# Optimization experiments

Hardware: AMD Instinct MI355X
Metric: run time of the kernel (lower is better)

The kernel has to match this reference:

```python
import jax, jax.numpy as jnp
import numpy as np

N, C1, C2, M, B, TOPK = 8192, 512, 128, 4, 256, 40
EPS = 1e-5


def setup_inputs() -> dict:
    key = jax.random.key(0)
    ks = jax.random.split(key, 8)
    s = 1.0 / np.sqrt(C2)
    return {
        "x": jax.random.normal(ks[0], (B, C1), jnp.float32),
        "embedding": jax.random.normal(ks[1], (N, C2), jnp.float32),
        "Wq": jax.random.uniform(ks[2], (M * C2, C2), jnp.float32, -s, s),
        "bq": jax.random.uniform(ks[3], (M * C2,), jnp.float32, -s, s),
        "Wv": jax.random.uniform(ks[4], (C2, C2), jnp.float32, -s, s),
        "bv": jax.random.uniform(ks[5], (C2,), jnp.float32, -s, s),
        "bn1_gamma": jnp.ones((C2,), jnp.float32),
        "bn1_beta": jnp.zeros((C2,), jnp.float32),
        "ln_gamma": jnp.ones((C2,), jnp.float32),
        "ln_beta": jnp.zeros((C2,), jnp.float32),
    }


def _perm_table():
    # torch.manual_seed(seed); torch.randperm(N) with seed in {0,1,2,3} ->
    # 4 fixed permutations. We use jax-native seeded permutations (same structure,
    # different concrete permutation values than torch's RNG).
    return jnp.stack([jax.random.permutation(jax.random.key(s), N) for s in range(4)])


def reference(x, embedding, Wq, bq, Wv, bv, bn1_gamma, bn1_beta, ln_gamma, ln_beta):
    # q path: [B, M, C2] -> to_q -> [B, M, M*C2] -> BN over C2 -> [B, M*M, C2]
    q = x.reshape(B, M, C2) @ Wq.T + bq                      # [B, M, M*C2]
    q = q.reshape(-1, C2)                                    # [B*M*M, C2]
    mu = q.mean(axis=0)
    var = q.var(axis=0)                                      # biased, like torch BN training
    q = (q - mu) / jnp.sqrt(var + EPS) * bn1_gamma + bn1_beta
    q = q.reshape(B, M * M, C2)

    v = embedding @ Wv.T + bv                                # [N, C2]
    kmu = embedding.mean(axis=-1, keepdims=True)
    kvar = embedding.var(axis=-1, keepdims=True)
    k = (embedding - kmu) / jnp.sqrt(kvar + EPS) * ln_gamma + ln_beta  # LN [N, C2]
    # torch does k.view(-1, c2, N) on contiguous [B, N, c2]: a raw RESHAPE, not transpose.
    k = k.reshape(C2, N)

    attn = jnp.einsum('bqc,cn->bqn', q, k) / jnp.sqrt(jnp.float32(C2))  # [B, M*M, N]
    attn = jax.nn.softmax(attn, axis=-1)
    applied = jnp.einsum('bqn,nc->bqc', attn, v)             # [B, M*M, C2]

    topv, topi = jax.lax.top_k(attn, TOPK)                   # [B, M*M, TOPK]
    bidx = jnp.arange(B)[:, None, None]
    qidx = jnp.arange(M * M)[None, :, None]
    masked = jnp.zeros_like(attn).at[bidx, qidx, topi].set(topv)

    avg = topi.reshape(B, -1).astype(jnp.float32).mean(axis=-1)
    seed = jnp.floor(avg / (N / 4.0)).astype(jnp.int32) % 4  # in {0..3}
    perms = _perm_table()[seed]                              # [B, N]
    idx = jnp.broadcast_to(perms[:, None, :], masked.shape)
    attn_w = jnp.take_along_axis(masked, idx, axis=-1)       # per-sample column permutation

    attn_w_flat = attn_w.reshape(B, -1)
    applied_flat = applied.reshape(B, -1)
    # matches torch return (attn_weights, x_s=[q, attn_applied], attn_applied)
    return attn_w_flat, q, applied, applied_flat
```

## Files before the change

### kernel.cpp

```cpp
#include <hip/hip_runtime.h>
#include <hip/hip_bf16.h>
#include <stdint.h>

#define EPSF 1e-5f

typedef __bf16 b16x8 __attribute__((ext_vector_type(8)));
typedef float f32x4 __attribute__((ext_vector_type(4)));
typedef unsigned short u16x8 __attribute__((ext_vector_type(8)));

static __device__ __forceinline__ unsigned short f2bf(float f) {
  __hip_bfloat16 h = __float2bfloat16(f);
  return __builtin_bit_cast(unsigned short, h);
}

__device__ __forceinline__ void threefry2x32(uint32_t k0, uint32_t k1,
                                             uint32_t c0, uint32_t c1,
                                             uint32_t& o0, uint32_t& o1) {
  const uint32_t ks2 = k0 ^ k1 ^ 0x1BD11BDAu;
  uint32_t x0 = c0 + k0, x1 = c1 + k1;
#define TFR(r) { x0 += x1; x1 = (x1 << (r)) | (x1 >> (32 - (r))); x1 ^= x0; }
  TFR(13) TFR(15) TFR(26) TFR(6)
  x0 += k1;  x1 += ks2 + 1u;
  TFR(17) TFR(29) TFR(16) TFR(24)
  x0 += ks2; x1 += k0 + 2u;
  TFR(13) TFR(15) TFR(26) TFR(6)
  x0 += k0;  x1 += k1 + 3u;
  TFR(17) TFR(29) TFR(16) TFR(24)
  x0 += k1;  x1 += ks2 + 4u;
  TFR(13) TFR(15) TFR(26) TFR(6)
  x0 += ks2; x1 += k0 + 5u;
#undef TFR
  o0 = x0; o1 = x1;
}

__global__ __launch_bounds__(256) void rank_kernel(int* __restrict__ rankbuf) {
  __shared__ uint32_t bits[8192];
  const int chunk = blockIdx.x;
  const int round = blockIdx.y;
  const int s     = blockIdx.z;
  const int t = threadIdx.x, l = t & 63, w = t >> 6;
  uint32_t ka, kb;
  {
    uint32_t k1a, k1b;
    threefry2x32(0u, (uint32_t)s, 0u, 0u, k1a, k1b);
    if (round == 0) threefry2x32(0u, (uint32_t)s, 0u, 1u, ka, kb);
    else            threefry2x32(k1a, k1b, 0u, 1u, ka, kb);
  }
  for (int j = t; j < 8192; j += 256) {
    uint32_t t0, t1;
    threefry2x32(ka, kb, 0u, (uint32_t)j, t0, t1);
    bits[j] = t1;
  }
  __syncthreads();
  const int base = chunk * 256 + w * 64;
  const int i = base + l;
  const uint32_t myb = bits[i];
  const uint4* b4 = (const uint4*)bits;
  int rk = 0;
  const int lo = base >> 2;
#pragma unroll 4
  for (int j4 = 0; j4 < lo; j4++) {
    const uint4 b = b4[j4];
    rk += (b.x <= myb) + (b.y <= myb) + (b.z <= myb) + (b.w <= myb);
  }
#pragma unroll
  for (int j4 = lo; j4 < lo + 16; j4++) {
    const uint4 b = b4[j4];
    const int j = j4 * 4;
    rk += (b.x < myb) + ((b.x == myb) && (j     < i));
    rk += (b.y < myb) + ((b.y == myb) && (j + 1 < i));
    rk += (b.z < myb) + ((b.z == myb) && (j + 2 < i));
    rk += (b.w < myb) + ((b.w == myb) && (j + 3 < i));
  }
#pragma unroll 4
  for (int j4 = lo + 16; j4 < 2048; j4++) {
    const uint4 b = b4[j4];
    rk += (b.x < myb) + (b.y < myb) + (b.z < myb) + (b.w < myb);
  }
  rankbuf[(s * 2 + round) * 8192 + i] = rk;
}

__global__ __launch_bounds__(256) void compose_kernel(const int* __restrict__ rankbuf,
                                                      int* __restrict__ invperm) {
  const int s = blockIdx.y;
  const int v = blockIdx.x * 256 + threadIdx.x;
  const int* r1 = rankbuf + s * 16384;
  const int* r2 = r1 + 8192;
  invperm[s * 8192 + v] = r2[r1[v]];
}

__global__ __launch_bounds__(256) void qraw_kernel(const float* __restrict__ x,
    const float* __restrict__ Wq, const float* __restrict__ bq,
    float* __restrict__ qraw) {
  __shared__ float ea[16][128];
  __shared__ float wq[128][132];
  const int t = threadIdx.x;
  const int g = blockIdx.x;
  const int m2 = blockIdx.y;
  for (int i = t; i < 512; i += 256) {
    float4 xx = *(const float4*)(x + (size_t)g * 2048 + i * 4);
    *(float4*)&ea[i >> 5][(i & 31) * 4] = xx;
  }
  for (int i = t; i < 4096; i += 256) {
    float4 ww = *(const float4*)(Wq + (size_t)m2 * 16384 + i * 4);
    *(float4*)&wq[i >> 5][(i & 31) * 4] = ww;
  }
  __syncthreads();
  const int row = t >> 4, j = t & 15;
  float acc[8] = {0.f,0.f,0.f,0.f,0.f,0.f,0.f,0.f};
  for (int d = 0; d < 128; d++) {
    const float xv = ea[row][d];
#pragma unroll
    for (int cc = 0; cc < 8; cc++) acc[cc] += xv * wq[j + cc * 16][d];
  }
  const int r = (g * 16 + row) * 4 + m2;
#pragma unroll
  for (int cc = 0; cc < 8; cc++) {
    const int c = j + cc * 16;
    qraw[(size_t)r * 128 + c] = acc[cc] + bq[m2 * 128 + c];
  }
}

__global__ __launch_bounds__(256) void bnpart_kernel(const float* __restrict__ qraw,
                                                     float* __restrict__ bnpart) {
  __shared__ float a1[256], a2[256];
  const int t = threadIdx.x, c = t & 127, h = t >> 7;
  float s1 = 0.f, s2 = 0.f;
  for (int i = 0; i < 64; i++) {
    float xv = qraw[(size_t)(blockIdx.x * 128 + h + 2 * i) * 128 + c];
    s1 += xv; s2 += xv * xv;
  }
  a1[t] = s1; a2[t] = s2;
  __syncthreads();
  if (t < 128) {
    bnpart[blockIdx.x * 256 + t]       = a1[t] + a1[t + 128];
    bnpart[blockIdx.x * 256 + 128 + t] = a2[t] + a2[t + 128];
  }
}

__global__ void bnfin_kernel(const float* __restrict__ bnpart,
                             const float* __restrict__ gamma,
                             const float* __restrict__ beta,
                             float* __restrict__ bnstat) {
  const int c = threadIdx.x;
  float s1 = 0.f, s2 = 0.f;
  for (int i = 0; i < 32; i++) { s1 += bnpart[i * 256 + c]; s2 += bnpart[i * 256 + 128 + c]; }
  const float mu  = s1 * (1.0f / 4096.0f);
  const float var = s2 * (1.0f / 4096.0f) - mu * mu;
  const float sc  = rsqrtf(var + EPSF) * gamma[c];
  bnstat[c]       = sc;
  bnstat[128 + c] = beta[c] - mu * sc;
}

__global__ __launch_bounds__(256) void qnorm_kernel(const float* __restrict__ qraw,
    const float* __restrict__ bnstat, float* __restrict__ outq,
    unsigned short* __restrict__ qb) {
  const int idx4 = blockIdx.x * 256 + threadIdx.x;
  float4 xv = *(const float4*)(qraw + (size_t)idx4 * 4);
  const int c0 = (idx4 * 4) & 127;
  float4 sc = *(const float4*)(bnstat + c0);
  float4 sh = *(const float4*)(bnstat + 128 + c0);
  float4 o;
  o.x = xv.x * sc.x + sh.x; o.y = xv.y * sc.y + sh.y;
  o.z = xv.z * sc.z + sh.z; o.w = xv.w * sc.w + sh.w;
  *(float4*)(outq + (size_t)idx4 * 4) = o;
  ushort4 ob;
  ob.x = f2bf(o.x); ob.y = f2bf(o.y); ob.z = f2bf(o.z); ob.w = f2bf(o.w);
  *(ushort4*)(qb + (size_t)idx4 * 4) = ob;
}

__global__ __launch_bounds__(256) void lnv_kernel(const float* __restrict__ emb,
    const float* __restrict__ Wv, const float* __restrict__ bv,
    const float* __restrict__ lng, const float* __restrict__ lnb,
    float* __restrict__ kbuf, float* __restrict__ vbuf) {
  __shared__ float ea[16][128];
  __shared__ float wv[128][132];
  const int t = threadIdx.x;
  const int r0 = blockIdx.x * 16;
  for (int i = t; i < 512; i += 256) {
    float4 xx = *(const float4*)(emb + (size_t)r0 * 128 + i * 4);
    *(float4*)&ea[i >> 5][(i & 31) * 4] = xx;
  }
  for (int i = t; i < 4096; i += 256) {
    float4 ww = *(const float4*)(Wv + (size_t)i * 4);
    *(float4*)&wv[i >> 5][(i & 31) * 4] = ww;
  }
  __syncthreads();
  const int row = t >> 4, j = t & 15;
  float s1 = 0.f, s2 = 0.f;
#pragma unroll
  for (int m = 0; m < 8; m++) { float xv = ea[row][j + m * 16]; s1 += xv; s2 += xv * xv; }
#pragma unroll
  for (int off = 8; off; off >>= 1) {
    s1 += __shfl_xor(s1, off, 16);
    s2 += __shfl_xor(s2, off, 16);
  }
  const float mu   = s1 * 0.0078125f;
  const float var  = s2 * 0.0078125f - mu * mu;
  const float rstd = rsqrtf(var + EPSF);
#pragma unroll
  for (int m = 0; m < 8; m++) {
    const int d = j + m * 16;
    kbuf[(size_t)(r0 + row) * 128 + d] = (ea[row][d] - mu) * rstd * lng[d] + lnb[d];
  }
  float acc[8] = {0.f,0.f,0.f,0.f,0.f,0.f,0.f,0.f};
  for (int d = 0; d < 128; d++) {
    const float xv = ea[row][d];
#pragma unroll
    for (int cc = 0; cc < 8; cc++) acc[cc] += xv * wv[j + cc * 16][d];
  }
#pragma unroll
  for (int cc = 0; cc < 8; cc++) {
    const int c = j + cc * 16;
    vbuf[(size_t)(r0 + row) * 128 + c] = acc[cc] + bv[c];
  }
}

__global__ __launch_bounds__(256) void ktrans_kernel(const float* __restrict__ kbuf,
                                                     unsigned short* __restrict__ kT) {
  __shared__ unsigned short s[64][136];
  const int b = blockIdx.x, t = threadIdx.x;
  const int k = t >> 1, half = t & 1;
  const float* src = kbuf + (size_t)(k * 64 + (b >> 1)) * 128 + (b & 1) * 64 + half * 32;
#pragma unroll
  for (int i = 0; i < 8; i++) {
    float4 v = *(const float4*)(src + i * 4);
    const int dn = half * 32 + i * 4;
    s[dn + 0][k] = f2bf(v.x); s[dn + 1][k] = f2bf(v.y);
    s[dn + 2][k] = f2bf(v.z); s[dn + 3][k] = f2bf(v.w);
  }
  __syncthreads();
  const int dn = t >> 2, q = t & 3;
  unsigned short* dst = kT + (size_t)(b * 64 + dn) * 128 + q * 32;
#pragma unroll
  for (int j = 0; j < 4; j++)
    *(int4*)(dst + j * 8) = *(const int4*)&s[dn][q * 32 + j * 8];
}

__global__ __launch_bounds__(256) void vtrans_kernel(const float* __restrict__ vbuf,
                                                     unsigned short* __restrict__ vT) {
  __shared__ unsigned short s[128][72];
  const int b = blockIdx.x, t = threadIdx.x;
  const int i0 = b * 64;
  const int di = t >> 2, q = t & 3;
  const float* src = vbuf + (size_t)(i0 + di) * 128 + q * 32;
#pragma unroll
  for (int i = 0; i < 8; i++) {
    float4 v = *(const float4*)(src + i * 4);
    const int c = q * 32 + i * 4;
    s[c + 0][di] = f2bf(v.x); s[c + 1][di] = f2bf(v.y);
    s[c + 2][di] = f2bf(v.z); s[c + 3][di] = f2bf(v.w);
  }
  __syncthreads();
  const int c = t >> 1, half = t & 1;
  unsigned short* dst = vT + (size_t)c * 8192 + i0 + half * 32;
#pragma unroll
  for (int j = 0; j < 4; j++)
    *(int4*)(dst + j * 8) = *(const int4*)&s[c][half * 32 + j * 8];
}

__global__ __launch_bounds__(256) void gemm1_mfma(const unsigned short* __restrict__ qb,
    const unsigned short* __restrict__ kT, float* __restrict__ logits) {
  __shared__ __attribute__((aligned(16))) unsigned short lds[32768];
  unsigned short* At = lds;
  unsigned short* Bt = lds + 16384;
  const int t = threadIdx.x, l = t & 63, w = t >> 6;
  const int n0 = blockIdx.x * 128, r0 = blockIdx.y * 128;
  const int wr = w >> 1, wc = w & 1;
#pragma unroll
  for (int it = 0; it < 8; it++) {
    const int c = it * 256 + t;
    const int row = c >> 4, ch = c & 15;
    const int chs = ch ^ (row & 7);
    const unsigned short* gA = qb + (size_t)(r0 + row) * 128 + chs * 8;
    const unsigned short* gB = kT + (size_t)(n0 + row) * 128 + chs * 8;
    __builtin_amdgcn_global_load_lds((const __attribute__((address_space(1))) void*)gA,
        (__attribute__((address_space(3))) void*)(At + (size_t)(it * 256 + w * 64) * 8), 16, 0, 0);
    __builtin_amdgcn_global_load_lds((const __attribute__((address_space(1))) void*)gB,
        (__attribute__((address_space(3))) void*)(Bt + (size_t)(it * 256 + w * 64) * 8), 16, 0, 0);
  }
  __syncthreads();
  f32x4 acc[4][4];
#pragma unroll
  for (int i = 0; i < 4; i++)
#pragma unroll
    for (int j = 0; j < 4; j++) acc[i][j] = (f32x4){0.f, 0.f, 0.f, 0.f};
#pragma unroll
  for (int ks = 0; ks < 4; ks++) {
    b16x8 af[4], bf[4];
#pragma unroll
    for (int i = 0; i < 4; i++) {
      const int rl = wr * 64 + i * 16 + (l & 15);
      const int ch = (ks * 4 + (l >> 4)) ^ (rl & 7);
      af[i] = __builtin_bit_cast(b16x8, *(const u16x8*)&At[rl * 128 + ch * 8]);
    }
#pragma unroll
    for (int j = 0; j < 4; j++) {
      const int cl = wc * 64 + j * 16 + (l & 15);
      const int ch = (ks * 4 + (l >> 4)) ^ (cl & 7);
      bf[j] = __builtin_bit_cast(b16x8, *(const u16x8*)&Bt[cl * 128 + ch * 8]);
    }
#pragma unroll
    for (int i = 0; i < 4; i++)
#pragma unroll
      for (int j = 0; j < 4; j++)
        acc[i][j] = __builtin_amdgcn_mfma_f32_16x16x32_bf16(af[i], bf[j], acc[i][j], 0, 0, 0);
  }
  __syncthreads();
  float* fb = (float*)lds;
  const float rs = 0.08838834764831845f;
#pragma unroll
  for (int i = 0; i < 4; i++)
#pragma unroll
    for (int j = 0; j < 4; j++) {
#pragma unroll
      for (int jj = 0; jj < 4; jj++) {
        const int row = wr * 64 + i * 16 + (l >> 4) * 4 + jj;
        const int col = wc * 64 + j * 16 + (l & 15);
        fb[row * 128 + col] = acc[i][j][jj] * rs;
      }
    }
  __syncthreads();
#pragma unroll
  for (int kk = 0; kk < 16; kk++) {
    const int idx4 = kk * 256 + t;
    const int row = idx4 >> 5, c4 = idx4 & 31;
    *(float4*)(logits + (size_t)(r0 + row) * 8192 + n0 + c4 * 4) = *(const float4*)&fb[row * 128 + c4 * 4];
  }
}

__global__ __launch_bounds__(256) void rowstat_topk_kernel(const float* __restrict__ logits,
    float* __restrict__ rowmax, float* __restrict__ rowsum,
    float* __restrict__ topv, int* __restrict__ topi) {
  const int r = blockIdx.x, t = threadIdx.x;
  const int l = t & 63, w = t >> 6;
  const float* row = logits + (size_t)r * 8192;
  float4 v[8];
#pragma unroll
  for (int m = 0; m < 8; m++) v[m] = *(const float4*)(row + m * 1024 + t * 4);

  __shared__ float sredf[4];
  __shared__ int scnt[16];
  __shared__ unsigned long long keys[1024];
  __shared__ int lcnt;

  float bm = -3.0e38f;
#pragma unroll
  for (int m = 0; m < 8; m++)
    bm = fmaxf(bm, fmaxf(fmaxf(v[m].x, v[m].y), fmaxf(v[m].z, v[m].w)));
#pragma unroll
  for (int off = 32; off; off >>= 1) bm = fmaxf(bm, __shfl_xor(bm, off));
  if (l == 0) sredf[w] = bm;
  __syncthreads();
  const float gmax = fmaxf(fmaxf(sredf[0], sredf[1]), fmaxf(sredf[2], sredf[3]));

  float ls = 0.f;
#pragma unroll
  for (int m = 0; m < 8; m++)
    ls += expf(v[m].x - gmax) + expf(v[m].y - gmax) + expf(v[m].z - gmax) + expf(v[m].w - gmax);
#pragma unroll
  for (int off = 32; off; off >>= 1) ls += __shfl_xor(ls, off);
  __syncthreads();
  if (l == 0) sredf[w] = ls;
  __syncthreads();
  const float gsum = sredf[0] + sredf[1] + sredf[2] + sredf[3];
  if (t == 0) { rowmax[r] = gmax; rowsum[r] = gsum; }

  float theta = -3.0e38f;
  bool found = false;
  for (int trial = 0; trial < 8 && !found; trial++) {
    const float base = gmax - 8.0f * (float)trial;
    int c[16];
#pragma unroll
    for (int j = 0; j < 16; j++) c[j] = 0;
#pragma unroll
    for (int m = 0; m < 8; m++) {
#pragma unroll
      for (int j = 0; j < 16; j++) {
        const float th = base - 0.5f * (float)(j + 1);
        c[j] += (v[m].x >= th) + (v[m].y >= th) + (v[m].z >= th) + (v[m].w >= th);
      }
    }
#pragma unroll
    for (int j = 0; j < 16; j++) {
#pragma unroll
      for (int off = 32; off; off >>= 1) c[j] += __shfl_xor(c[j], off);
    }
    if (t < 16) scnt[t] = 0;
    __syncthreads();
    if (l == 0) {
#pragma unroll
      for (int j = 0; j < 16; j++) atomicAdd(&scnt[j], c[j]);
    }
    __syncthreads();
    for (int j = 0; j < 16; j++) {
      if (scnt[j] >= 40) { theta = base - 0.5f * (float)(j + 1); found = true; break; }
    }
    __syncthreads();
  }

  if (t == 0) lcnt = 0;
  __syncthreads();
#pragma unroll
  for (int m = 0; m < 8; m++) {
    const int gb = m * 1024 + t * 4;
    const float vals[4] = {v[m].x, v[m].y, v[m].z, v[m].w};
#pragma unroll
    for (int e = 0; e < 4; e++) {
      if (vals[e] >= theta) {
        const int pos = atomicAdd(&lcnt, 1);
        if (pos < 1024) {
          const uint32_t s = __float_as_uint(vals[e]);
          const uint32_t mkey = (s & 0x80000000u) ? ~s : (s | 0x80000000u);
          keys[pos] = ((unsigned long long)(~mkey) << 32) | (unsigned)(gb + e);
        }
      }
    }
  }
  __syncthreads();
  const int cnt = min(lcnt, 1024);
  const float rgs = 1.0f / gsum;
  for (int i = t; i < cnt; i += 256) {
    const unsigned long long K = keys[i];
    int rank = 0;
#pragma unroll 4
    for (int p = 0; p < cnt; p++) rank += (keys[p] < K) ? 1 : 0;
    if (rank < 40) {
      const uint32_t desc = (uint32_t)(K >> 32);
      const uint32_t mkey = ~desc;
      const uint32_t sb = (mkey & 0x80000000u) ? (mkey & 0x7FFFFFFFu) : ~mkey;
      const float val = __uint_as_float(sb);
      topi[r * 40 + rank] = (int)(K & 0xFFFFFFFFu);
      topv[r * 40 + rank] = expf(val - gmax) * rgs;
    }
  }
}

__global__ __launch_bounds__(256) void gemm2_mfma(const float* __restrict__ logits,
    const unsigned short* __restrict__ vT, const float* __restrict__ rowmax,
    const float* __restrict__ rowsum, float* __restrict__ pvpart) {
  __shared__ __attribute__((aligned(16))) unsigned short lds[32768];
  unsigned short* At = lds;
  unsigned short* Bt = lds + 8192;
  const int t = threadIdx.x, l = t & 63, w = t >> 6;
  const int bx = blockIdx.x;
  const int by = blockIdx.y;
  const int r0 = by * 128;
  const int kb0 = bx * 1024;
  const int wr = w >> 1, wc = w & 1;
  const int prow = t >> 1, pk = (t & 1) * 32;
  const float rm = rowmax[r0 + prow];
  const float ri = 1.0f / rowsum[r0 + prow];

  f32x4 acc[4][4];
#pragma unroll
  for (int i = 0; i < 4; i++)
#pragma unroll
    for (int j = 0; j < 4; j++) acc[i][j] = (f32x4){0.f, 0.f, 0.f, 0.f};

  for (int ks = 0; ks < 16; ks++) {
    const int k0 = kb0 + ks * 64;
    __syncthreads();
#pragma unroll
    for (int it = 0; it < 4; it++) {
      const int c = it * 256 + t;
      const int rowc = c >> 3, ch = c & 7;
      const int chs = ch ^ (rowc & 7);
      const unsigned short* gB = vT + (size_t)rowc * 8192 + k0 + chs * 8;
      __builtin_amdgcn_global_load_lds((const __attribute__((address_space(1))) void*)gB,
          (__attribute__((address_space(3))) void*)(Bt + (size_t)(it * 256 + w * 64) * 8), 16, 0, 0);
    }
    const float* lsrc = logits + (size_t)(r0 + prow) * 8192 + k0 + pk;
#pragma unroll
    for (int c8 = 0; c8 < 4; c8++) {
      float4 v0 = *(const float4*)(lsrc + c8 * 8);
      float4 v1 = *(const float4*)(lsrc + c8 * 8 + 4);
      u16x8 pkd;
      pkd[0] = f2bf(expf(v0.x - rm) * ri); pkd[1] = f2bf(expf(v0.y - rm) * ri);
      pkd[2] = f2bf(expf(v0.z - rm) * ri); pkd[3] = f2bf(expf(v0.w - rm) * ri);
      pkd[4] = f2bf(expf(v1.x - rm) * ri); pkd[5] = f2bf(expf(v1.y - rm) * ri);
      pkd[6] = f2bf(expf(v1.z - rm) * ri); pkd[7] = f2bf(expf(v1.w - rm) * ri);
      const int chunkidx = (t & 1) * 4 + c8;
      const int phys = chunkidx ^ (prow & 7);
      *(u16x8*)&At[prow * 64 + phys * 8] = pkd;
    }
    __syncthreads();
#pragma unroll
    for (int s = 0; s < 2; s++) {
      b16x8 af[4], bf[4];
#pragma unroll
      for (int i = 0; i < 4; i++) {
        const int rl = wr * 64 + i * 16 + (l & 15);
        const int ch = (s * 4 + (l >> 4)) ^ (rl & 7);
        af[i] = __builtin_bit_cast(b16x8, *(const u16x8*)&At[rl * 64 + ch * 8]);
      }
#pragma unroll
      for (int j = 0; j < 4; j++) {
        const int cl = wc * 64 + j * 16 + (l & 15);
        const int ch = (s * 4 + (l >> 4)) ^ (cl & 7);
        bf[j] = __builtin_bit_cast(b16x8, *(const u16x8*)&Bt[cl * 64 + ch * 8]);
      }
#pragma unroll
      for (int i = 0; i < 4; i++)
#pragma unroll
        for (int j = 0; j < 4; j++)
          acc[i][j] = __builtin_amdgcn_mfma_f32_16x16x32_bf16(af[i], bf[j], acc[i][j], 0, 0, 0);
    }
  }
  __syncthreads();
  float* fb = (float*)lds;
#pragma unroll
  for (int i = 0; i < 4; i++)
#pragma unroll
    for (int j = 0; j < 4; j++)
#pragma unroll
      for (int jj = 0; jj < 4; jj++) {
        const int row = wr * 64 + i * 16 + (l >> 4) * 4 + jj;
        const int col = wc * 64 + j * 16 + (l & 15);
        fb[row * 128 + col] = acc[i][j][jj];
      }
  __syncthreads();
#pragma unroll
  for (int kk = 0; kk < 16; kk++) {
    const int idx4 = kk * 256 + t;
    const int row = idx4 >> 5, c4 = idx4 & 31;
    *(float4*)(pvpart + ((size_t)bx * 4096 + r0 + row) * 128 + c4 * 4) = *(const float4*)&fb[row * 128 + c4 * 4];
  }
}

__global__ __launch_bounds__(256) void pvred_kernel(const float* __restrict__ pvpart,
    float* __restrict__ o2, float* __restrict__ o3) {
  const int idx4 = blockIdx.x * 256 + threadIdx.x;
  float4 s; s.x = s.y = s.z = s.w = 0.f;
#pragma unroll
  for (int ch = 0; ch < 8; ch++) {
    float4 p = *(const float4*)(pvpart + (size_t)ch * 524288 + (size_t)idx4 * 4);
    s.x += p.x; s.y += p.y; s.z += p.z; s.w += p.w;
  }
  *(float4*)(o2 + (size_t)idx4 * 4) = s;
  *(float4*)(o3 + (size_t)idx4 * 4) = s;
}

__global__ __launch_bounds__(256) void seedscatter_kernel(const int* __restrict__ topi,
    const float* __restrict__ topv, const int* __restrict__ invperm,
    float* __restrict__ out0) {
  const int b = blockIdx.x, t = threadIdx.x;
  int s = 0;
  for (int e = t; e < 640; e += 256) s += topi[b * 640 + e];
#pragma unroll
  for (int off = 32; off; off >>= 1) s += __shfl_xor(s, off);
  __shared__ int sred[4];
  if ((t & 63) == 0) sred[t >> 6] = s;
  __syncthreads();
  const int total = sred[0] + sred[1] + sred[2] + sred[3];
  const float avg = (float)total / 640.0f;
  const int sd = ((int)floorf(avg / 2048.0f)) & 3;
  const int* ip = invperm + sd * 8192;
  for (int e = t; e < 640; e += 256) {
    const int q = e / 40;
    const int i = topi[b * 640 + e];
    const float val = topv[b * 640 + e];
    out0[((size_t)(b * 16 + q)) * 8192 + ip[i]] = val;
  }
}

extern "C" void kernel_launch(void* const* d_in, const int* in_sizes, int n_in,
                              void* d_out, int out_size, void* d_ws, size_t ws_size,
                              hipStream_t stream) {
  const float* x   = (const float*)d_in[0];
  const float* emb = (const float*)d_in[1];
  const float* Wq  = (const float*)d_in[2];
  const float* bq  = (const float*)d_in[3];
  const float* Wv  = (const float*)d_in[4];
  const float* bv  = (const float*)d_in[5];
  const float* bng = (const float*)d_in[6];
  const float* bnb = (const float*)d_in[7];
  const float* lng = (const float*)d_in[8];
  const float* lnb = (const float*)d_in[9];

  float* out0  = (float*)d_out;
  float* outq  = out0 + 33554432;
  float* outap = outq + 524288;
  float* outaf = outap + 524288;

  float* wsf    = (float*)d_ws;
  float* kbuf   = wsf;
  float* vbuf   = kbuf + 1048576;
  float* qraw   = vbuf + 1048576;
  float* bnpart = qraw + 524288;
  float* bnstat = bnpart + 8192;
  float* rowmax = bnstat + 256;
  float* rowsum = rowmax + 4096;
  float* pvpart = rowsum + 4096;
  float* topv   = pvpart + 4194304;
  int*   topi    = (int*)(topv + 163840);
  int*   invperm = topi + 163840;
  int*   rankbuf = invperm + 32768;
  unsigned short* qb = (unsigned short*)(rankbuf + 65536);
  unsigned short* kT = qb + 524288;
  unsigned short* vT = kT + 1048576;

  rank_kernel<<<dim3(32, 2, 4), 256, 0, stream>>>(rankbuf);
  compose_kernel<<<dim3(32, 4), 256, 0, stream>>>(rankbuf, invperm);
  qraw_kernel<<<dim3(64, 4), 256, 0, stream>>>(x, Wq, bq, qraw);
  bnpart_kernel<<<32, 256, 0, stream>>>(qraw, bnpart);
  bnfin_kernel<<<1, 128, 0, stream>>>(bnpart, bng, bnb, bnstat);
  qnorm_kernel<<<512, 256, 0, stream>>>(qraw, bnstat, outq, qb);
  lnv_kernel<<<512, 256, 0, stream>>>(emb, Wv, bv, lng, lnb, kbuf, vbuf);
  ktrans_kernel<<<128, 256, 0, stream>>>(kbuf, kT);
  vtrans_kernel<<<128, 256, 0, stream>>>(vbuf, vT);
  gemm1_mfma<<<dim3(64, 32), 256, 0, stream>>>(qb, kT, out0);
  rowstat_topk_kernel<<<4096, 256, 0, stream>>>(out0, rowmax, rowsum, topv, topi);
  gemm2_mfma<<<dim3(8, 32), 256, 0, stream>>>(out0, vT, rowmax, rowsum, pvpart);
  pvred_kernel<<<512, 256, 0, stream>>>(pvpart, outap, outaf);
  hipMemsetAsync(d_out, 0, (size_t)33554432 * 4, stream);
  seedscatter_kernel<<<256, 256, 0, stream>>>(topi, topv, invperm, out0);
}
```

Measured before the change: 419.2 us.

## Fuse QK logits, softmax, PV and top-k candidate collection into flash-style kernels

```diff
diff --git a/kernel.cpp b/kernel.cpp
--- a/kernel.cpp
+++ b/kernel.cpp
@@ -3,6 +3,7 @@
 #include <stdint.h>
 
 #define EPSF 1e-5f
+#define RSQ 0.08838834764831845f
 
 typedef __bf16 b16x8 __attribute__((ext_vector_type(8)));
 typedef float f32x4 __attribute__((ext_vector_type(4)));
@@ -11,6 +12,9 @@
 static __device__ __forceinline__ unsigned short f2bf(float f) {
   __hip_bfloat16 h = __float2bfloat16(f);
   return __builtin_bit_cast(unsigned short, h);
+}
+static __device__ __forceinline__ float bf2f(unsigned short u) {
+  union { unsigned int i; float f; } x; x.i = ((unsigned int)u) << 16; return x.f;
 }
 
 __device__ __forceinline__ void threefry2x32(uint32_t k0, uint32_t k1,
@@ -216,327 +220,440 @@
   }
 }
 
-__global__ __launch_bounds__(256) void ktrans_kernel(const float* __restrict__ kbuf,
-                                                     unsigned short* __restrict__ kT) {
-  __shared__ unsigned short s[64][136];
+__global__ __launch_bounds__(256) void kvtrans_kernel(const float* __restrict__ kbuf,
+    const float* __restrict__ vbuf, unsigned short* __restrict__ kT,
+    unsigned short* __restrict__ vT) {
+  __shared__ __attribute__((aligned(16))) unsigned short sbuf[9216];
   const int b = blockIdx.x, t = threadIdx.x;
-  const int k = t >> 1, half = t & 1;
-  const float* src = kbuf + (size_t)(k * 64 + (b >> 1)) * 128 + (b & 1) * 64 + half * 32;
-#pragma unroll
-  for (int i = 0; i < 8; i++) {
-    float4 v = *(const float4*)(src + i * 4);
-    const int dn = half * 32 + i * 4;
-    s[dn + 0][k] = f2bf(v.x); s[dn + 1][k] = f2bf(v.y);
-    s[dn + 2][k] = f2bf(v.z); s[dn + 3][k] = f2bf(v.w);
-  }
-  __syncthreads();
-  const int dn = t >> 2, q = t & 3;
-  unsigned short* dst = kT + (size_t)(b * 64 + dn) * 128 + q * 32;
-#pragma unroll
-  for (int j = 0; j < 4; j++)
-    *(int4*)(dst + j * 8) = *(const int4*)&s[dn][q * 32 + j * 8];
-}
-
-__global__ __launch_bounds__(256) void vtrans_kernel(const float* __restrict__ vbuf,
-                                                     unsigned short* __restrict__ vT) {
-  __shared__ unsigned short s[128][72];
-  const int b = blockIdx.x, t = threadIdx.x;
-  const int i0 = b * 64;
-  const int di = t >> 2, q = t & 3;
-  const float* src = vbuf + (size_t)(i0 + di) * 128 + q * 32;
-#pragma unroll
-  for (int i = 0; i < 8; i++) {
-    float4 v = *(const float4*)(src + i * 4);
-    const int c = q * 32 + i * 4;
-    s[c + 0][di] = f2bf(v.x); s[c + 1][di] = f2bf(v.y);
-    s[c + 2][di] = f2bf(v.z); s[c + 3][di] = f2bf(v.w);
-  }
-  __syncthreads();
-  const int c = t >> 1, half = t & 1;
-  unsigned short* dst = vT + (size_t)c * 8192 + i0 + half * 32;
-#pragma unroll
-  for (int j = 0; j < 4; j++)
-    *(int4*)(dst + j * 8) = *(const int4*)&s[c][half * 32 + j * 8];
-}
-
-__global__ __launch_bounds__(256) void gemm1_mfma(const unsigned short* __restrict__ qb,
-    const unsigned short* __restrict__ kT, float* __restrict__ logits) {
+  if (blockIdx.y == 0) {
+    unsigned short (*s)[136] = (unsigned short (*)[136])sbuf;
+    const int k = t >> 1, half = t & 1;
+    const float* src = kbuf + (size_t)(k * 64 + (b >> 1)) * 128 + (b & 1) * 64 + half * 32;
+#pragma unroll
+    for (int i = 0; i < 8; i++) {
+      float4 v = *(const float4*)(src + i * 4);
+      const int dn = half * 32 + i * 4;
+      s[dn + 0][k] = f2bf(v.x); s[dn + 1][k] = f2bf(v.y);
+      s[dn + 2][k] = f2bf(v.z); s[dn + 3][k] = f2bf(v.w);
+    }
+    __syncthreads();
+    const int dn = t >> 2, q = t & 3;
+    unsigned short* dst = kT + (size_t)(b * 64 + dn) * 128 + q * 32;
+#pragma unroll
+    for (int j = 0; j < 4; j++)
+      *(int4*)(dst + j * 8) = *(const int4*)&s[dn][q * 32 + j * 8];
+  } else {
+    unsigned short (*s)[72] = (unsigned short (*)[72])sbuf;
+    const int i0 = b * 64;
+    const int di = t >> 2, q = t & 3;
+    const float* src = vbuf + (size_t)(i0 + di) * 128 + q * 32;
+#pragma unroll
+    for (int i = 0; i < 8; i++) {
+      float4 v = *(const float4*)(src + i * 4);
+      const int c = q * 32 + i * 4;
+      s[c + 0][di] = f2bf(v.x); s[c + 1][di] = f2bf(v.y);
+      s[c + 2][di] = f2bf(v.z); s[c + 3][di] = f2bf(v.w);
+    }
+    __syncthreads();
+    const int c = t >> 1, half = t & 1;
+    unsigned short* dst = vT + (size_t)c * 8192 + i0 + half * 32;
+#pragma unroll
+    for (int j = 0; j < 4; j++)
+      *(int4*)(dst + j * 8) = *(const int4*)&s[c][half * 32 + j * 8];
+  }
+}
+
+__global__ __launch_bounds__(512) void stats1_kernel(const unsigned short* __restrict__ qb,
+    const unsigned short* __restrict__ kT, float* __restrict__ maxpart) {
+  __shared__ __attribute__((aligned(16))) unsigned short ktt[16384];
+  __shared__ float red[128][4];
+  const int t = threadIdx.x, l = t & 63, w = t >> 6;
+  const int bx = blockIdx.x;
+  const int r0 = blockIdx.y * 128;
+  const int n0 = bx * 1024;
+  const int wr = w >> 2, wcol = w & 3;
+  b16x8 afr[4][4];
+#pragma unroll
+  for (int i = 0; i < 4; i++) {
+    const int rl = r0 + wr * 64 + i * 16 + (l & 15);
+#pragma unroll
+    for (int ks = 0; ks < 4; ks++)
+      afr[i][ks] = __builtin_bit_cast(b16x8,
+          *(const u16x8*)(qb + (size_t)rl * 128 + ks * 32 + (l >> 4) * 8));
+  }
+  float m16[4][4];
+#pragma unroll
+  for (int i = 0; i < 4; i++)
+#pragma unroll
+    for (int jj = 0; jj < 4; jj++) m16[i][jj] = -3.0e38f;
+
+  for (int ct = 0; ct < 8; ct++) {
+    __syncthreads();
+#pragma unroll
+    for (int it = 0; it < 4; it++) {
+      const int c = it * 512 + t;
+      const int row = c >> 4, ch = c & 15;
+      const int chs = ch ^ (row & 7);
+      const unsigned short* g = kT + (size_t)(n0 + ct * 128 + row) * 128 + chs * 8;
+      __builtin_amdgcn_global_load_lds((const __attribute__((address_space(1))) void*)g,
+          (__attribute__((address_space(3))) void*)(ktt + (size_t)(it * 512 + w * 64) * 8), 16, 0, 0);
+    }
+    __syncthreads();
+    f32x4 sacc[4][2];
+#pragma unroll
+    for (int i = 0; i < 4; i++)
+#pragma unroll
+      for (int j = 0; j < 2; j++) sacc[i][j] = (f32x4){0.f, 0.f, 0.f, 0.f};
+#pragma unroll
+    for (int ks = 0; ks < 4; ks++) {
+      b16x8 bf[2];
+#pragma unroll
+      for (int j = 0; j < 2; j++) {
+        const int cl = wcol * 32 + j * 16 + (l & 15);
+        const int ch = (ks * 4 + (l >> 4)) ^ (cl & 7);
+        bf[j] = __builtin_bit_cast(b16x8, *(const u16x8*)&ktt[cl * 128 + ch * 8]);
+      }
+#pragma unroll
+      for (int i = 0; i < 4; i++)
+#pragma unroll
+        for (int j = 0; j < 2; j++)
+          sacc[i][j] = __builtin_amdgcn_mfma_f32_16x16x32_bf16(afr[i][ks], bf[j], sacc[i][j], 0, 0, 0);
+    }
+#pragma unroll
+    for (int i = 0; i < 4; i++)
+#pragma unroll
+      for (int jj = 0; jj < 4; jj++)
+        m16[i][jj] = fmaxf(m16[i][jj], fmaxf(sacc[i][0][jj], sacc[i][1][jj]));
+  }
+#pragma unroll
+  for (int i = 0; i < 4; i++)
+#pragma unroll
+    for (int jj = 0; jj < 4; jj++) {
+      float m = m16[i][jj];
+#pragma unroll
+      for (int off = 8; off; off >>= 1) m = fmaxf(m, __shfl_xor(m, off));
+      if ((l & 15) == 0) red[wr * 64 + i * 16 + (l >> 4) * 4 + jj][wcol] = m;
+    }
+  __syncthreads();
+  if (t < 128)
+    maxpart[bx * 4096 + r0 + t] =
+        fmaxf(fmaxf(red[t][0], red[t][1]), fmaxf(red[t][2], red[t][3]));
+}
+
+__global__ __launch_bounds__(256) void rowmax_fin_kernel(const float* __restrict__ maxpart,
+                                                         float* __restrict__ rowmax) {
+  const int idx = blockIdx.x * 256 + threadIdx.x;
+  float m = -3.0e38f;
+#pragma unroll
+  for (int c = 0; c < 8; c++) m = fmaxf(m, maxpart[c * 4096 + idx]);
+  rowmax[idx] = m * RSQ;
+}
+
+__global__ __launch_bounds__(512) void fused2_kernel(const unsigned short* __restrict__ qb,
+    const unsigned short* __restrict__ kT, const unsigned short* __restrict__ vT,
+    const float* __restrict__ rowmax, float* __restrict__ pvpart,
+    float* __restrict__ expsumpart, unsigned long long* __restrict__ candbuf,
+    int* __restrict__ cnt) {
   __shared__ __attribute__((aligned(16))) unsigned short lds[32768];
-  unsigned short* At = lds;
-  unsigned short* Bt = lds + 16384;
+  unsigned short* kvt = lds;
+  unsigned short* pt  = lds + 16384;
   const int t = threadIdx.x, l = t & 63, w = t >> 6;
-  const int n0 = blockIdx.x * 128, r0 = blockIdx.y * 128;
-  const int wr = w >> 1, wc = w & 1;
-#pragma unroll
-  for (int it = 0; it < 8; it++) {
-    const int c = it * 256 + t;
-    const int row = c >> 4, ch = c & 15;
-    const int chs = ch ^ (row & 7);
-    const unsigned short* gA = qb + (size_t)(r0 + row) * 128 + chs * 8;
-    const unsigned short* gB = kT + (size_t)(n0 + row) * 128 + chs * 8;
-    __builtin_amdgcn_global_load_lds((const __attribute__((address_space(1))) void*)gA,
-        (__attribute__((address_space(3))) void*)(At + (size_t)(it * 256 + w * 64) * 8), 16, 0, 0);
-    __builtin_amdgcn_global_load_lds((const __attribute__((address_space(1))) void*)gB,
-        (__attribute__((address_space(3))) void*)(Bt + (size_t)(it * 256 + w * 64) * 8), 16, 0, 0);
-  }
-  __syncthreads();
-  f32x4 acc[4][4];
+  const int bx = blockIdx.x;
+  const int r0 = blockIdx.y * 128;
+  const int n0 = bx * 1024;
+  const int wr = w >> 2, wcol = w & 3;
+  b16x8 afr[4][4];
+#pragma unroll
+  for (int i = 0; i < 4; i++) {
+    const int rl = r0 + wr * 64 + i * 16 + (l & 15);
+#pragma unroll
+    for (int ks = 0; ks < 4; ks++)
+      afr[i][ks] = __builtin_bit_cast(b16x8,
+          *(const u16x8*)(qb + (size_t)rl * 128 + ks * 32 + (l >> 4) * 8));
+  }
+  float rm16[4][4], es16[4][4];
 #pragma unroll
   for (int i = 0; i < 4; i++)
 #pragma unroll
-    for (int j = 0; j < 4; j++) acc[i][j] = (f32x4){0.f, 0.f, 0.f, 0.f};
-#pragma unroll
-  for (int ks = 0; ks < 4; ks++) {
-    b16x8 af[4], bf[4];
-#pragma unroll
-    for (int i = 0; i < 4; i++) {
-      const int rl = wr * 64 + i * 16 + (l & 15);
-      const int ch = (ks * 4 + (l >> 4)) ^ (rl & 7);
-      af[i] = __builtin_bit_cast(b16x8, *(const u16x8*)&At[rl * 128 + ch * 8]);
-    }
-#pragma unroll
-    for (int j = 0; j < 4; j++) {
-      const int cl = wc * 64 + j * 16 + (l & 15);
-      const int ch = (ks * 4 + (l >> 4)) ^ (cl & 7);
-      bf[j] = __builtin_bit_cast(b16x8, *(const u16x8*)&Bt[cl * 128 + ch * 8]);
-    }
+    for (int jj = 0; jj < 4; jj++) {
+      rm16[i][jj] = rowmax[r0 + wr * 64 + i * 16 + (l >> 4) * 4 + jj];
+      es16[i][jj] = 0.f;
+    }
+  f32x4 pv[4][2];
+#pragma unroll
+  for (int i = 0; i < 4; i++)
+#pragma unroll
+    for (int j = 0; j < 2; j++) pv[i][j] = (f32x4){0.f, 0.f, 0.f, 0.f};
+
+  for (int ct = 0; ct < 8; ct++) {
+    __syncthreads();
+#pragma unroll
+    for (int it = 0; it < 4; it++) {
+      const int c = it * 512 + t;
+      const int row = c >> 4, ch = c & 15;
+      const int chs = ch ^ (row & 7);
+      const unsigned short* g = kT + (size_t)(n0 + ct * 128 + row) * 128 + chs * 8;
+      __builtin_amdgcn_global_load_lds((const __attribute__((address_space(1))) void*)g,
+          (__attribute__((address_space(3))) void*)(kvt + (size_t)(it * 512 + w * 64) * 8), 16, 0, 0);
+    }
+    __syncthreads();
+    f32x4 sacc[4][2];
 #pragma unroll
     for (int i = 0; i < 4; i++)
 #pragma unroll
-      for (int j = 0; j < 4; j++)
-        acc[i][j] = __builtin_amdgcn_mfma_f32_16x16x32_bf16(af[i], bf[j], acc[i][j], 0, 0, 0);
-  }
-  __syncthreads();
-  float* fb = (float*)lds;
-  const float rs = 0.08838834764831845f;
-#pragma unroll
-  for (int i = 0; i < 4; i++)
-#pragma unroll
-    for (int j = 0; j < 4; j++) {
-#pragma unroll
-      for (int jj = 0; jj < 4; jj++) {
-        const int row = wr * 64 + i * 16 + (l >> 4) * 4 + jj;
-        const int col = wc * 64 + j * 16 + (l & 15);
-        fb[row * 128 + col] = acc[i][j][jj] * rs;
+      for (int j = 0; j < 2; j++) sacc[i][j] = (f32x4){0.f, 0.f, 0.f, 0.f};
+#pragma unroll
+    for (int ks = 0; ks < 4; ks++) {
+      b16x8 bf[2];
+#pragma unroll
+      for (int j = 0; j < 2; j++) {
+        const int cl = wcol * 32 + j * 16 + (l & 15);
+        const int ch = (ks * 4 + (l >> 4)) ^ (cl & 7);
+        bf[j] = __builtin_bit_cast(b16x8, *(const u16x8*)&kvt[cl * 128 + ch * 8]);
       }
-    }
-  __syncthreads();
-#pragma unroll
-  for (int kk = 0; kk < 16; kk++) {
-    const int idx4 = kk * 256 + t;
-    const int row = idx4 >> 5, c4 = idx4 & 31;
-    *(float4*)(logits + (size_t)(r0 + row) * 8192 + n0 + c4 * 4) = *(const float4*)&fb[row * 128 + c4 * 4];
-  }
-}
-
-__global__ __launch_bounds__(256) void rowstat_topk_kernel(const float* __restrict__ logits,
-    float* __restrict__ rowmax, float* __restrict__ rowsum,
-    float* __restrict__ topv, int* __restrict__ topi) {
-  const int r = blockIdx.x, t = threadIdx.x;
-  const int l = t & 63, w = t >> 6;
-  const float* row = logits + (size_t)r * 8192;
-  float4 v[8];
-#pragma unroll
-  for (int m = 0; m < 8; m++) v[m] = *(const float4*)(row + m * 1024 + t * 4);
-
-  __shared__ float sredf[4];
-  __shared__ int scnt[16];
-  __shared__ unsigned long long keys[1024];
-  __shared__ int lcnt;
-
-  float bm = -3.0e38f;
-#pragma unroll
-  for (int m = 0; m < 8; m++)
-    bm = fmaxf(bm, fmaxf(fmaxf(v[m].x, v[m].y), fmaxf(v[m].z, v[m].w)));
-#pragma unroll
-  for (int off = 32; off; off >>= 1) bm = fmaxf(bm, __shfl_xor(bm, off));
-  if (l == 0) sredf[w] = bm;
-  __syncthreads();
-  const float gmax = fmaxf(fmaxf(sredf[0], sredf[1]), fmaxf(sredf[2], sredf[3]));
-
-  float ls = 0.f;
-#pragma unroll
-  for (int m = 0; m < 8; m++)
-    ls += expf(v[m].x - gmax) + expf(v[m].y - gmax) + expf(v[m].z - gmax) + expf(v[m].w - gmax);
-#pragma unroll
-  for (int off = 32; off; off >>= 1) ls += __shfl_xor(ls, off);
-  __syncthreads();
-  if (l == 0) sredf[w] = ls;
-  __syncthreads();
-  const float gsum = sredf[0] + sredf[1] + sredf[2] + sredf[3];
-  if (t == 0) { rowmax[r] = gmax; rowsum[r] = gsum; }
-
-  float theta = -3.0e38f;
-  bool found = false;
-  for (int trial = 0; trial < 8 && !found; trial++) {
-    const float base = gmax - 8.0f * (float)trial;
-    int c[16];
-#pragma unroll
-    for (int j = 0; j < 16; j++) c[j] = 0;
-#pragma unroll
-    for (int m = 0; m < 8; m++) {
-#pragma unroll
-      for (int j = 0; j < 16; j++) {
-        const float th = base - 0.5f * (float)(j + 1);
-        c[j] += (v[m].x >= th) + (v[m].y >= th) + (v[m].z >= th) + (v[m].w >= th);
-      }
-    }
-#pragma unroll
-    for (int j = 0; j < 16; j++) {
-#pragma unroll
-      for (int off = 32; off; off >>= 1) c[j] += __shfl_xor(c[j], off);
-    }
-    if (t < 16) scnt[t] = 0;
-    __syncthreads();
-    if (l == 0) {
-#pragma unroll
-      for (int j = 0; j < 16; j++) atomicAdd(&scnt[j], c[j]);
-    }
-    __syncthreads();
-    for (int j = 0; j < 16; j++) {
-      if (scnt[j] >= 40) { theta = base - 0.5f * (float)(j + 1); found = true; break; }
-    }
-    __syncthreads();
-  }
-
-  if (t == 0) lcnt = 0;
-  __syncthreads();
-#pragma unroll
-  for (int m = 0; m < 8; m++) {
-    const int gb = m * 1024 + t * 4;
-    const float vals[4] = {v[m].x, v[m].y, v[m].z, v[m].w};
-#pragma unroll
-    for (int e = 0; e < 4; e++) {
-      if (vals[e] >= theta) {
-        const int pos = atomicAdd(&lcnt, 1);
-        if (pos < 1024) {
-          const uint32_t s = __float_as_uint(vals[e]);
-          const uint32_t mkey = (s & 0x80000000u) ? ~s : (s | 0x80000000u);
-          keys[pos] = ((unsigned long long)(~mkey) << 32) | (unsigned)(gb + e);
+#pragma unroll
+      for (int i = 0; i < 4; i++)
+#pragma unroll
+        for (int j = 0; j < 2; j++)
+          sacc[i][j] = __builtin_amdgcn_mfma_f32_16x16x32_bf16(afr[i][ks], bf[j], sacc[i][j], 0, 0, 0);
+    }
+#pragma unroll
+    for (int i = 0; i < 4; i++)
+#pragma unroll
+      for (int j = 0; j < 2; j++) {
+        const int colb = wcol * 32 + j * 16 + (l & 15);
+#pragma unroll
+        for (int jj = 0; jj < 4; jj++) {
+          const int prow = wr * 64 + i * 16 + (l >> 4) * 4 + jj;
+          const float logit = sacc[i][j][jj] * RSQ;
+          const float p = expf(logit - rm16[i][jj]);
+          es16[i][jj] += p;
+          const int physc = (((colb >> 3) ^ (prow & 7)) << 3) + (colb & 7);
+          pt[prow * 128 + physc] = f2bf(p);
+          if (logit >= rm16[i][jj] - 2.0f) {
+            const int rg = r0 + prow;
+            const int pos = atomicAdd(&cnt[rg * 8 + bx], 1);
+            if (pos < 160) {
+              const uint32_t sb = __float_as_uint(logit);
+              const uint32_t mk = (sb & 0x80000000u) ? ~sb : (sb | 0x80000000u);
+              candbuf[((size_t)rg * 8 + bx) * 160 + pos] =
+                  ((unsigned long long)(~mk) << 32) | (unsigned)(n0 + ct * 128 + colb);
+            }
+          }
         }
       }
-    }
-  }
-  __syncthreads();
-  const int cnt = min(lcnt, 1024);
-  const float rgs = 1.0f / gsum;
-  for (int i = t; i < cnt; i += 256) {
+    __syncthreads();
+#pragma unroll
+    for (int it = 0; it < 4; it++) {
+      const int c = it * 512 + t;
+      const int row = c >> 4, ch = c & 15;
+      const int chs = ch ^ (row & 7);
+      const unsigned short* g = vT + (size_t)row * 8192 + n0 + ct * 128 + chs * 8;
+      __builtin_amdgcn_global_load_lds((const __attribute__((address_space(1))) void*)g,
+          (__attribute__((address_space(3))) void*)(kvt + (size_t)(it * 512 + w * 64) * 8), 16, 0, 0);
+    }
+    __syncthreads();
+#pragma unroll
+    for (int ks = 0; ks < 4; ks++) {
+      b16x8 paf[4], vbf[2];
+#pragma unroll
+      for (int i = 0; i < 4; i++) {
+        const int rl = wr * 64 + i * 16 + (l & 15);
+        const int ch = (ks * 4 + (l >> 4)) ^ (rl & 7);
+        paf[i] = __builtin_bit_cast(b16x8, *(const u16x8*)&pt[rl * 128 + ch * 8]);
+      }
+#pragma unroll
+      for (int j = 0; j < 2; j++) {
+        const int cl = wcol * 32 + j * 16 + (l & 15);
+        const int ch = (ks * 4 + (l >> 4)) ^ (cl & 7);
+        vbf[j] = __builtin_bit_cast(b16x8, *(const u16x8*)&kvt[cl * 128 + ch * 8]);
+      }
+#pragma unroll
+      for (int i = 0; i < 4; i++)
+#pragma unroll
+        for (int j = 0; j < 2; j++)
+          pv[i][j] = __builtin_amdgcn_mfma_f32_16x16x32_bf16(paf[i], vbf[j], pv[i][j], 0, 0, 0);
+    }
+  }
+  __syncthreads();
+  float* red = (float*)lds;
+#pragma unroll
+  for (int i = 0; i < 4; i++)
+#pragma unroll
+    for (int jj = 0; jj < 4; jj++) {
+      float e = es16[i][jj];
+#pragma unroll
+      for (int off = 8; off; off >>= 1) e += __shfl_xor(e, off);
+      if ((l & 15) == 0) red[(wr * 64 + i * 16 + (l >> 4) * 4 + jj) * 4 + wcol] = e;
+    }
+  __syncthreads();
+  if (t < 128)
+    expsumpart[bx * 4096 + r0 + t] = red[t * 4] + red[t * 4 + 1] + red[t * 4 + 2] + red[t * 4 + 3];
+  __syncthreads();
+  float* fb = (float*)lds;
+#pragma unroll
+  for (int i = 0; i < 4; i++)
+#pragma unroll
+    for (int j = 0; j < 2; j++)
+#pragma unroll
+      for (int jj = 0; jj < 4; jj++)
+        fb[(wr * 64 + i * 16 + (l >> 4) * 4 + jj) * 128 + wcol * 32 + j * 16 + (l & 15)] = pv[i][j][jj];
+  __syncthreads();
+#pragma unroll
+  for (int kk = 0; kk < 8; kk++) {
+    const int idx4 = kk * 512 + t;
+    const int row = idx4 >> 5, c4 = idx4 & 31;
+    *(float4*)(pvpart + ((size_t)bx * 4096 + r0 + row) * 128 + c4 * 4) = *(const float4*)&fb[row * 128 + c4 * 4];
+  }
+}
+
+__global__ __launch_bounds__(256) void rank40_kernel(const int* __restrict__ cnt,
+    const unsigned long long* __restrict__ candbuf, const float* __restrict__ rowmax,
+    const float* __restrict__ expsumpart, float* __restrict__ topv, int* __restrict__ topi) {
+  __shared__ unsigned long long keys[1280];
+  __shared__ int bases[9];
+  __shared__ int okflag;
+  const int r = blockIdx.x, t = threadIdx.x;
+  if (t == 0) {
+    int tot = 0, ok = 1;
+    for (int c = 0; c < 8; c++) {
+      bases[c] = tot;
+      const int n = cnt[r * 8 + c];
+      if (n > 160) ok = 0;
+      tot += (n > 160 ? 160 : n);
+    }
+    bases[8] = tot;
+    okflag = (ok && tot >= 40) ? tot : 0;
+  }
+  __syncthreads();
+  const int total = okflag;
+  if (total == 0) return;
+#pragma unroll
+  for (int c = 0; c < 8; c++) {
+    const int b0 = bases[c], n = bases[c + 1] - b0;
+    for (int i = t; i < n; i += 256) keys[b0 + i] = candbuf[((size_t)r * 8 + c) * 160 + i];
+  }
+  __syncthreads();
+  float gsum = 0.f;
+#pragma unroll
+  for (int c = 0; c < 8; c++) gsum += expsumpart[c * 4096 + r];
+  const float rm = rowmax[r], rgs = 1.0f / gsum;
+  for (int i = t; i < total; i += 256) {
     const unsigned long long K = keys[i];
     int rank = 0;
 #pragma unroll 4
-    for (int p = 0; p < cnt; p++) rank += (keys[p] < K) ? 1 : 0;
+    for (int p = 0; p < total; p++) rank += (keys[p] < K) ? 1 : 0;
     if (rank < 40) {
       const uint32_t desc = (uint32_t)(K >> 32);
-      const uint32_t mkey = ~desc;
-      const uint32_t sb = (mkey & 0x80000000u) ? (mkey & 0x7FFFFFFFu) : ~mkey;
-      const float val = __uint_as_float(sb);
+      const uint32_t mk = ~desc;
+      const uint32_t sb = (mk & 0x80000000u) ? (mk & 0x7FFFFFFFu) : ~mk;
       topi[r * 40 + rank] = (int)(K & 0xFFFFFFFFu);
-      topv[r * 40 + rank] = expf(val - gmax) * rgs;
-    }
-  }
-}
-
-__global__ __launch_bounds__(256) void gemm2_mfma(const float* __restrict__ logits,
-    const unsigned short* __restrict__ vT, const float* __restrict__ rowmax,
-    const float* __restrict__ rowsum, float* __restrict__ pvpart) {
-  __shared__ __attribute__((aligned(16))) unsigned short lds[32768];
-  unsigned short* At = lds;
-  unsigned short* Bt = lds + 8192;
-  const int t = threadIdx.x, l = t & 63, w = t >> 6;
-  const int bx = blockIdx.x;
-  const int by = blockIdx.y;
-  const int r0 = by * 128;
-  const int kb0 = bx * 1024;
-  const int wr = w >> 1, wc = w & 1;
-  const int prow = t >> 1, pk = (t & 1) * 32;
-  const float rm = rowmax[r0 + prow];
-  const float ri = 1.0f / rowsum[r0 + prow];
-
-  f32x4 acc[4][4];
-#pragma unroll
-  for (int i = 0; i < 4; i++)
-#pragma unroll
-    for (int j = 0; j < 4; j++) acc[i][j] = (f32x4){0.f, 0.f, 0.f, 0.f};
-
-  for (int ks = 0; ks < 16; ks++) {
-    const int k0 = kb0 + ks * 64;
-    __syncthreads();
-#pragma unroll
-    for (int it = 0; it < 4; it++) {
-      const int c = it * 256 + t;
-      const int rowc = c >> 3, ch = c & 7;
-      const int chs = ch ^ (rowc & 7);
-      const unsigned short* gB = vT + (size_t)rowc * 8192 + k0 + chs * 8;
-      __builtin_amdgcn_global_load_lds((const __attribute__((address_space(1))) void*)gB,
-          (__attribute__((address_space(3))) void*)(Bt + (size_t)(it * 256 + w * 64) * 8), 16, 0, 0);
-    }
-    const float* lsrc = logits + (size_t)(r0 + prow) * 8192 + k0 + pk;
-#pragma unroll
-    for (int c8 = 0; c8 < 4; c8++) {
-      float4 v0 = *(const float4*)(lsrc + c8 * 8);
-      float4 v1 = *(const float4*)(lsrc + c8 * 8 + 4);
-      u16x8 pkd;
-      pkd[0] = f2bf(expf(v0.x - rm) * ri); pkd[1] = f2bf(expf(v0.y - rm) * ri);
-      pkd[2] = f2bf(expf(v0.z - rm) * ri); pkd[3] = f2bf(expf(v0.w - rm) * ri);
-      pkd[4] = f2bf(expf(v1.x - rm) * ri); pkd[5] = f2bf(expf(v1.y - rm) * ri);
-      pkd[6] = f2bf(expf(v1.z - rm) * ri); pkd[7] = f2bf(expf(v1.w - rm) * ri);
-      const int chunkidx = (t & 1) * 4 + c8;
-      const int phys = chunkidx ^ (prow & 7);
-      *(u16x8*)&At[prow * 64 + phys * 8] = pkd;
-    }
-    __syncthreads();
-#pragma unroll
-    for (int s = 0; s < 2; s++) {
-      b16x8 af[4], bf[4];
-#pragma unroll
-      for (int i = 0; i < 4; i++) {
-        const int rl = wr * 64 + i * 16 + (l & 15);
-        const int ch = (s * 4 + (l >> 4)) ^ (rl & 7);
-        af[i] = __builtin_bit_cast(b16x8, *(const u16x8*)&At[rl * 64 + ch * 8]);
+      topv[r * 40 + rank] = expf(__uint_as_float(sb) - rm) * rgs;
+    }
+  }
+}
+
+__global__ __launch_bounds__(256) void repair_kernel(const int* __restrict__ cnt,
+    const unsigned short* __restrict__ qb, const unsigned short* __restrict__ kT,
+    const float* __restrict__ rowmax, const float* __restrict__ expsumpart,
+    float* __restrict__ topv, int* __restrict__ topi) {
+  const int r = blockIdx.x, t = threadIdx.x, l = t & 63, w = t >> 6;
+  __shared__ int need;
+  if (t == 0) {
+    int tot = 0, ok = 1;
+    for (int c = 0; c < 8; c++) {
+      const int n = cnt[r * 8 + c];
+      if (n > 160) ok = 0;
+      tot += (n > 160 ? 160 : n);
+    }
+    need = (ok && tot >= 40) ? 0 : 1;
+  }
+  __syncthreads();
+  if (!need) return;
+  __shared__ float lg[8192];
+  __shared__ float qrow[128];
+  __shared__ float sred[4];
+  __shared__ int scnt;
+  __shared__ unsigned long long keys[2048];
+  __shared__ int lc;
+  if (t < 128) qrow[t] = bf2f(qb[(size_t)r * 128 + t]);
+  __syncthreads();
+  for (int j = t; j < 8192; j += 256) {
+    float acc = 0.f;
+    const unsigned short* kr = kT + (size_t)j * 128;
+    for (int k = 0; k < 128; k++) acc += qrow[k] * bf2f(kr[k]);
+    lg[j] = acc * RSQ;
+  }
+  __syncthreads();
+  float bm = -3.0e38f;
+  for (int j = t; j < 8192; j += 256) bm = fmaxf(bm, lg[j]);
+#pragma unroll
+  for (int off = 32; off; off >>= 1) bm = fmaxf(bm, __shfl_xor(bm, off));
+  if (l == 0) sred[w] = bm;
+  __syncthreads();
+  bm = fmaxf(fmaxf(sred[0], sred[1]), fmaxf(sred[2], sred[3]));
+  float theta = bm;
+  for (int trial = 0; trial < 32; trial++) {
+    theta = bm - 0.6f * (float)(trial + 1);
+    int c = 0;
+    for (int j = t; j < 8192; j += 256) c += (lg[j] >= theta) ? 1 : 0;
+#pragma unroll
+    for (int off = 32; off; off >>= 1) c += __shfl_xor(c, off);
+    __syncthreads();
+    if (t == 0) scnt = 0;
+    __syncthreads();
+    if (l == 0) atomicAdd(&scnt, c);
+    __syncthreads();
+    if (scnt >= 40) break;
+  }
+  if (t == 0) lc = 0;
+  __syncthreads();
+  for (int j = t; j < 8192; j += 256) {
+    const float v = lg[j];
+    if (v >= theta) {
+      const int pos = atomicAdd(&lc, 1);
+      if (pos < 2048) {
+        const uint32_t sb = __float_as_uint(v);
+        const uint32_t mk = (sb & 0x80000000u) ? ~sb : (sb | 0x80000000u);
+        keys[pos] = ((unsigned long long)(~mk) << 32) | (unsigned)j;
       }
-#pragma unroll
-      for (int j = 0; j < 4; j++) {
-        const int cl = wc * 64 + j * 16 + (l & 15);
-        const int ch = (s * 4 + (l >> 4)) ^ (cl & 7);
-        bf[j] = __builtin_bit_cast(b16x8, *(const u16x8*)&Bt[cl * 64 + ch * 8]);
-      }
-#pragma unroll
-      for (int i = 0; i < 4; i++)
-#pragma unroll
-        for (int j = 0; j < 4; j++)
-          acc[i][j] = __builtin_amdgcn_mfma_f32_16x16x32_bf16(af[i], bf[j], acc[i][j], 0, 0, 0);
-    }
-  }
-  __syncthreads();
-  float* fb = (float*)lds;
-#pragma unroll
-  for (int i = 0; i < 4; i++)
-#pragma unroll
-    for (int j = 0; j < 4; j++)
-#pragma unroll
-      for (int jj = 0; jj < 4; jj++) {
-        const int row = wr * 64 + i * 16 + (l >> 4) * 4 + jj;
-        const int col = wc * 64 + j * 16 + (l & 15);
-        fb[row * 128 + col] = acc[i][j][jj];
-      }
-  __syncthreads();
-#pragma unroll
-  for (int kk = 0; kk < 16; kk++) {
-    const int idx4 = kk * 256 + t;
-    const int row = idx4 >> 5, c4 = idx4 & 31;
-    *(float4*)(pvpart + ((size_t)bx * 4096 + r0 + row) * 128 + c4 * 4) = *(const float4*)&fb[row * 128 + c4 * 4];
+    }
+  }
+  __syncthreads();
+  const int total = min(lc, 2048);
+  float gsum = 0.f;
+#pragma unroll
+  for (int c = 0; c < 8; c++) gsum += expsumpart[c * 4096 + r];
+  const float rm = rowmax[r], rgs = 1.0f / gsum;
+  for (int i = t; i < total; i += 256) {
+    const unsigned long long K = keys[i];
+    int rank = 0;
+    for (int p = 0; p < total; p++) rank += (keys[p] < K) ? 1 : 0;
+    if (rank < 40) {
+      const uint32_t desc = (uint32_t)(K >> 32);
+      const uint32_t mk = ~desc;
+      const uint32_t sb = (mk & 0x80000000u) ? (mk & 0x7FFFFFFFu) : ~mk;
+      topi[r * 40 + rank] = (int)(K & 0xFFFFFFFFu);
+      topv[r * 40 + rank] = expf(__uint_as_float(sb) - rm) * rgs;
+    }
   }
 }
 
 __global__ __launch_bounds__(256) void pvred_kernel(const float* __restrict__ pvpart,
-    float* __restrict__ o2, float* __restrict__ o3) {
+    const float* __restrict__ expsumpart, float* __restrict__ o2, float* __restrict__ o3) {
   const int idx4 = blockIdx.x * 256 + threadIdx.x;
+  const int row = idx4 >> 5;
+  float gs = 0.f;
+#pragma unroll
+  for (int c = 0; c < 8; c++) gs += expsumpart[c * 4096 + row];
+  const float ri = 1.0f / gs;
   float4 s; s.x = s.y = s.z = s.w = 0.f;
 #pragma unroll
   for (int ch = 0; ch < 8; ch++) {
     float4 p = *(const float4*)(pvpart + (size_t)ch * 524288 + (size_t)idx4 * 4);
     s.x += p.x; s.y += p.y; s.z += p.z; s.w += p.w;
   }
+  s.x *= ri; s.y *= ri; s.z *= ri; s.w *= ri;
   *(float4*)(o2 + (size_t)idx4 * 4) = s;
   *(float4*)(o3 + (size_t)idx4 * 4) = s;
 }
@@ -583,23 +700,28 @@
   float* outap = outq + 524288;
   float* outaf = outap + 524288;
 
-  float* wsf    = (float*)d_ws;
-  float* kbuf   = wsf;
-  float* vbuf   = kbuf + 1048576;
-  float* qraw   = vbuf + 1048576;
-  float* bnpart = qraw + 524288;
-  float* bnstat = bnpart + 8192;
-  float* rowmax = bnstat + 256;
-  float* rowsum = rowmax + 4096;
-  float* pvpart = rowsum + 4096;
-  float* topv   = pvpart + 4194304;
-  int*   topi    = (int*)(topv + 163840);
-  int*   invperm = topi + 163840;
-  int*   rankbuf = invperm + 32768;
+  float* wsf        = (float*)d_ws;
+  float* kbuf       = wsf;
+  float* vbuf       = kbuf + 1048576;
+  float* qraw       = vbuf + 1048576;
+  float* bnpart     = qraw + 524288;
+  float* bnstat     = bnpart + 8192;
+  float* rowmax     = bnstat + 256;
+  float* maxpart    = rowmax + 4096;
+  float* expsumpart = maxpart + 32768;
+  float* pvpart     = expsumpart + 32768;
+  float* topv       = pvpart + 4194304;
+  int*   topi       = (int*)(topv + 163840);
+  int*   cnt        = topi + 163840;
+  int*   invperm    = cnt + 32768;
+  int*   rankbuf    = invperm + 32768;
   unsigned short* qb = (unsigned short*)(rankbuf + 65536);
   unsigned short* kT = qb + 524288;
   unsigned short* vT = kT + 1048576;
-
+  unsigned long long* candbuf = (unsigned long long*)(vT + 1048576);
+
+  hipMemsetAsync(out0, 0, (size_t)33554432 * 4, stream);
+  hipMemsetAsync(cnt, 0, (size_t)32768 * 4, stream);
   rank_kernel<<<dim3(32, 2, 4), 256, 0, stream>>>(rankbuf);
   compose_kernel<<<dim3(32, 4), 256, 0, stream>>>(rankbuf, invperm);
   qraw_kernel<<<dim3(64, 4), 256, 0, stream>>>(x, Wq, bq, qraw);
@@ -607,12 +729,13 @@
   bnfin_kernel<<<1, 128, 0, stream>>>(bnpart, bng, bnb, bnstat);
   qnorm_kernel<<<512, 256, 0, stream>>>(qraw, bnstat, outq, qb);
   lnv_kernel<<<512, 256, 0, stream>>>(emb, Wv, bv, lng, lnb, kbuf, vbuf);
-  ktrans_kernel<<<128, 256, 0, stream>>>(kbuf, kT);
-  vtrans_kernel<<<128, 256, 0, stream>>>(vbuf, vT);
-  gemm1_mfma<<<dim3(64, 32), 256, 0, stream>>>(qb, kT, out0);
-  rowstat_topk_kernel<<<4096, 256, 0, stream>>>(out0, rowmax, rowsum, topv, topi);
-  gemm2_mfma<<<dim3(8, 32), 256, 0, stream>>>(out0, vT, rowmax, rowsum, pvpart);
-  pvred_kernel<<<512, 256, 0, stream>>>(pvpart, outap, outaf);
-  hipMemsetAsync(d_out, 0, (size_t)33554432 * 4, stream);
+  kvtrans_kernel<<<dim3(128, 2), 256, 0, stream>>>(kbuf, vbuf, kT, vT);
+  stats1_kernel<<<dim3(8, 32), 512, 0, stream>>>(qb, kT, maxpart);
+  rowmax_fin_kernel<<<16, 256, 0, stream>>>(maxpart, rowmax);
+  fused2_kernel<<<dim3(8, 32), 512, 0, stream>>>(qb, kT, vT, rowmax, pvpart,
+                                                 expsumpart, candbuf, cnt);
+  rank40_kernel<<<4096, 256, 0, stream>>>(cnt, candbuf, rowmax, expsumpart, topv, topi);
+  repair_kernel<<<4096, 256, 0, stream>>>(cnt, qb, kT, rowmax, expsumpart, topv, topi);
+  pvred_kernel<<<512, 256, 0, stream>>>(pvpart, expsumpart, outap, outaf);
   seedscatter_kernel<<<256, 256, 0, stream>>>(topi, topv, invperm, out0);
 }
```

After: 884.9 us. +111.1%, slower.
